# Performance work log

Hardware: AMD Instinct MI355X
Metric: run time of the kernel (lower is better)

## Reference

```python
import jax, jax.numpy as jnp
import numpy as np

EPS = 1e-09  # present in module but unused in forward math

def setup_inputs() -> dict:
    key = jax.random.key(0)
    k1, k2 = jax.random.split(key)
    n, d = 4096, 512
    outputs = jax.random.normal(k1, (n, d), dtype=jnp.float32)
    labels = jax.random.randint(k2, (n,), 0, 100, dtype=jnp.int64)
    return {"outputs": outputs, "labels": labels, "margin": 1.0}

def reference(outputs, labels, margin):
    # Pairwise squared L2 distances D[i,j] = ||x_i - x_j||^2 via expansion.
    sq = jnp.sum(outputs * outputs, axis=-1)                     # [n]
    D = sq[:, None] + sq[None, :] - 2.0 * (outputs @ outputs.T)  # [n, n]
    D = jnp.maximum(D, 0.0)
    same = (labels[:, None] == labels[None, :])                  # [n, n] bool; includes diagonal
    zn1 = jnp.sum(same)
    zn2 = same.size - zn1
    sum1 = jnp.sum(jnp.where(same, D, 0.0))
    sum2 = jnp.sum(jnp.where(same, 0.0, jnp.maximum(0.0, margin - D)))
    return 0.5 * (sum1 / zn1 + sum2 / zn2)
```

## Files before the change

kernel.cpp:

```cpp
#include <hip/hip_runtime.h>
#include <stdint.h>

#define NROWS 4096
#define DIM   512
#define BK    32
#define TILE  128
#define NBLK  32
#define NPAIR 528
#define KT    (DIM / BK)

typedef float f32x4 __attribute__((ext_vector_type(4)));
typedef short s16x8 __attribute__((ext_vector_type(8)));

#define OFF_XB   0u
#define OFF_SQ   (NROWS * DIM * 2u)
#define OFF_LAB  (OFF_SQ + NROWS * 4u)
#define OFF_ACC  (OFF_LAB + NROWS * 4u)

__device__ __forceinline__ unsigned short f2bf(float f) {
  unsigned u = __float_as_uint(f);
  return (unsigned short)((u + 0x7FFFu + ((u >> 16) & 1u)) >> 16);
}

typedef __attribute__((address_space(1))) unsigned int glb_uint;
typedef __attribute__((address_space(3))) unsigned int lds_uint;

__device__ __forceinline__ void gl2lds16(const void* g, void* l) {
  __builtin_amdgcn_global_load_lds(
      (glb_uint*)(uintptr_t)g,
      (lds_uint*)(unsigned int)(uintptr_t)l,
      16, 0, 0);
}

__global__ __launch_bounds__(256) void prep_kernel(
    const float* __restrict__ X, const long long* __restrict__ lab,
    unsigned short* __restrict__ Xb, float* __restrict__ sq,
    int* __restrict__ labi, float* __restrict__ accum)
{
  int t = threadIdx.x;
  int gid = blockIdx.x * 256 + t;
  if (gid < 4) accum[gid] = 0.0f;
  if (gid < NROWS) labi[gid] = (int)lab[gid];

  int wave = t >> 6, lane = t & 63;
  int row = blockIdx.x * 4 + wave;
  const float4* Xr = (const float4*)(X + (size_t)row * DIM);
  float4 a = Xr[lane * 2];
  float4 b = Xr[lane * 2 + 1];

  uint4 pk;
  pk.x = (unsigned)f2bf(a.x) | ((unsigned)f2bf(a.y) << 16);
  pk.y = (unsigned)f2bf(a.z) | ((unsigned)f2bf(a.w) << 16);
  pk.z = (unsigned)f2bf(b.x) | ((unsigned)f2bf(b.y) << 16);
  pk.w = (unsigned)f2bf(b.z) | ((unsigned)f2bf(b.w) << 16);
  *(uint4*)(Xb + (size_t)row * DIM + lane * 8) = pk;

  float s = a.x*a.x + a.y*a.y + a.z*a.z + a.w*a.w
          + b.x*b.x + b.y*b.y + b.z*b.z + b.w*b.w;
  #pragma unroll
  for (int off = 32; off; off >>= 1) s += __shfl_down(s, off, 64);
  if (lane == 0) sq[row] = s;
}

__global__ __launch_bounds__(256) void pair_kernel(
    const unsigned short* __restrict__ Xb, const float* __restrict__ sq,
    const int* __restrict__ labi, const float* __restrict__ marginp,
    float* __restrict__ accum, float* __restrict__ out)
{
  __shared__ unsigned short As[2][TILE * BK];
  __shared__ unsigned short Bs[2][TILE * BK];
  __shared__ float sRow[TILE], sCol[TILE];
  __shared__ int   lRow[TILE], lCol[TILE];
  __shared__ float rs1[4], rs2[4];
  __shared__ int   rc[4];

  int t = threadIdx.x;

  int rem = blockIdx.x, bi = 0;
  while (rem >= (NBLK - bi)) { rem -= (NBLK - bi); bi++; }
  int bj = bi + rem;

  if (t < TILE) {
    sRow[t] = sq[bi * TILE + t];
    lRow[t] = labi[bi * TILE + t];
  } else {
    int u = t - TILE;
    sCol[u] = sq[bj * TILE + u];
    lCol[u] = labi[bj * TILE + u];
  }

  int wave = t >> 6, lane = t & 63;
  int quad = lane >> 4, ml = lane & 15;
  int waveRow = (wave >> 1) * 64, waveCol = (wave & 1) * 64;

  f32x4 acc[4][4] = {};

  const int r0 = t >> 2;
  const int g  = (t & 3) ^ ((t >> 3) & 3);
  const size_t gA0 = (size_t)(bi * TILE +      r0) * DIM + g * 8;
  const size_t gA1 = (size_t)(bi * TILE + 64 + r0) * DIM + g * 8;
  const size_t gB0 = (size_t)(bj * TILE +      r0) * DIM + g * 8;
  const size_t gB1 = (size_t)(bj * TILE + 64 + r0) * DIM + g * 8;
  const int ldst = t * 8;

  const int slot = quad ^ ((ml >> 1) & 3);

  gl2lds16(Xb + gA0, (void*)(As[0] + ldst));
  gl2lds16(Xb + gA1, (void*)(As[0] + 2048 + ldst));
  gl2lds16(Xb + gB0, (void*)(Bs[0] + ldst));
  gl2lds16(Xb + gB1, (void*)(Bs[0] + 2048 + ldst));

  for (int kt = 0; kt < KT; ++kt) {
    int cur = kt & 1;
    __syncthreads();

    if (kt + 1 < KT) {
      size_t ko = (size_t)(kt + 1) * BK;
      gl2lds16(Xb + gA0 + ko, (void*)(As[cur ^ 1] + ldst));
      gl2lds16(Xb + gA1 + ko, (void*)(As[cur ^ 1] + 2048 + ldst));
      gl2lds16(Xb + gB0 + ko, (void*)(Bs[cur ^ 1] + ldst));
      gl2lds16(Xb + gB1 + ko, (void*)(Bs[cur ^ 1] + 2048 + ldst));
    }

    const s16x8* Ap = (const s16x8*)As[cur];
    const s16x8* Bp = (const s16x8*)Bs[cur];
    s16x8 af[4], bfr[4];
    #pragma unroll
    for (int r = 0; r < 4; ++r) {
      int row = waveRow + r * 16 + ml;
      af[r] = Ap[row * 4 + slot];
    }
    #pragma unroll
    for (int c = 0; c < 4; ++c) {
      int col = waveCol + c * 16 + ml;
      bfr[c] = Bp[col * 4 + slot];
    }

    #pragma unroll
    for (int r = 0; r < 4; ++r)
      #pragma unroll
      for (int c = 0; c < 4; ++c)
        acc[r][c] = __builtin_amdgcn_mfma_f32_16x16x32_bf16(af[r], bfr[c], acc[r][c], 0, 0, 0);
  }

  float margin = *marginp;
  float s1 = 0.f, s2 = 0.f;
  int cnt = 0;
  #pragma unroll
  for (int c = 0; c < 4; ++c) {
    int col = waveCol + c * 16 + ml;
    float sqc = sCol[col];
    int lc = lCol[col];
    #pragma unroll
    for (int r = 0; r < 4; ++r) {
      int rbase = waveRow + r * 16 + quad * 4;
      #pragma unroll
      for (int i = 0; i < 4; ++i) {
        int row = rbase + i;
        float d = sRow[row] + sqc - 2.0f * acc[r][c][i];
        d = fmaxf(d, 0.0f);
        if (lRow[row] == lc) { s1 += d; cnt++; }
        else                 { s2 += fmaxf(margin - d, 0.0f); }
      }
    }
  }

  #pragma unroll
  for (int off = 32; off; off >>= 1) {
    s1  += __shfl_down(s1, off, 64);
    s2  += __shfl_down(s2, off, 64);
    cnt += __shfl_down(cnt, off, 64);
  }
  if (lane == 0) { rs1[wave] = s1; rs2[wave] = s2; rc[wave] = cnt; }
  __syncthreads();
  if (t == 0) {
    float f = (bi == bj) ? 1.f : 2.f;
    float S1 = 0.f, S2 = 0.f;
    int C = 0;
    for (int w = 0; w < 4; ++w) { S1 += rs1[w]; S2 += rs2[w]; C += rc[w]; }
    atomicAdd(&accum[0], S1 * f);
    atomicAdd(&accum[1], S2 * f);
    atomicAdd((unsigned*)accum + 2, (unsigned)C * (unsigned)((bi == bj) ? 1 : 2));
    __threadfence();
    unsigned prev = atomicAdd((unsigned*)accum + 3, 1u);
    if (prev == NPAIR - 1) {
      float s1v = atomicAdd(&accum[0], 0.0f);
      float s2v = atomicAdd(&accum[1], 0.0f);
      unsigned c1 = atomicAdd((unsigned*)accum + 2, 0u);
      double zn1 = (double)c1;
      double zn2 = (double)NROWS * (double)NROWS - zn1;
      out[0] = (float)(0.5 * ((double)s1v / zn1 + (double)s2v / zn2));
    }
  }
}

extern "C" void kernel_launch(void* const* d_in, const int* in_sizes, int n_in,
                              void* d_out, int out_size, void* d_ws, size_t ws_size,
                              hipStream_t stream) {
  const float*     X      = (const float*)d_in[0];
  const long long* lab    = (const long long*)d_in[1];
  const float*     margin = (const float*)d_in[2];
  float*           out    = (float*)d_out;

  char* ws = (char*)d_ws;
  unsigned short* Xb   = (unsigned short*)(ws + OFF_XB);
  float*          sq   = (float*)(ws + OFF_SQ);
  int*            labi = (int*)(ws + OFF_LAB);
  float*          accum= (float*)(ws + OFF_ACC);

  prep_kernel<<<NROWS / 4, 256, 0, stream>>>(X, lab, Xb, sq, labi, accum);
  pair_kernel<<<NPAIR, 256, 0, stream>>>(Xb, sq, labi, margin, accum, out);
}
```

Baseline: 102.8 us.

## Load MFMA fragments directly from global memory and switch to fp16 inputs

```diff
diff --git a/kernel.cpp b/kernel.cpp
--- a/kernel.cpp
+++ b/kernel.cpp
@@ -1,40 +1,25 @@
 #include <hip/hip_runtime.h>
+#include <hip/hip_fp16.h>
 #include <stdint.h>
 
 #define NROWS 4096
 #define DIM   512
-#define BK    32
 #define TILE  128
 #define NBLK  32
 #define NPAIR 528
-#define KT    (DIM / BK)
+#define KSTEPS 16
 
-typedef float f32x4 __attribute__((ext_vector_type(4)));
-typedef short s16x8 __attribute__((ext_vector_type(8)));
+typedef float    f32x4 __attribute__((ext_vector_type(4)));
+typedef _Float16 f16x8 __attribute__((ext_vector_type(8)));
 
-#define OFF_XB   0u
+#define OFF_XH   0u
 #define OFF_SQ   (NROWS * DIM * 2u)
 #define OFF_LAB  (OFF_SQ + NROWS * 4u)
 #define OFF_ACC  (OFF_LAB + NROWS * 4u)
 
-__device__ __forceinline__ unsigned short f2bf(float f) {
-  unsigned u = __float_as_uint(f);
-  return (unsigned short)((u + 0x7FFFu + ((u >> 16) & 1u)) >> 16);
-}
-
-typedef __attribute__((address_space(1))) unsigned int glb_uint;
-typedef __attribute__((address_space(3))) unsigned int lds_uint;
-
-__device__ __forceinline__ void gl2lds16(const void* g, void* l) {
-  __builtin_amdgcn_global_load_lds(
-      (glb_uint*)(uintptr_t)g,
-      (lds_uint*)(unsigned int)(uintptr_t)l,
-      16, 0, 0);
-}
-
 __global__ __launch_bounds__(256) void prep_kernel(
     const float* __restrict__ X, const long long* __restrict__ lab,
-    unsigned short* __restrict__ Xb, float* __restrict__ sq,
+    unsigned short* __restrict__ Xh, float* __restrict__ sq,
     int* __restrict__ labi, float* __restrict__ accum)
 {
   int t = threadIdx.x;
@@ -49,11 +34,11 @@
   float4 b = Xr[lane * 2 + 1];
 
   uint4 pk;
-  pk.x = (unsigned)f2bf(a.x) | ((unsigned)f2bf(a.y) << 16);
-  pk.y = (unsigned)f2bf(a.z) | ((unsigned)f2bf(a.w) << 16);
-  pk.z = (unsigned)f2bf(b.x) | ((unsigned)f2bf(b.y) << 16);
-  pk.w = (unsigned)f2bf(b.z) | ((unsigned)f2bf(b.w) << 16);
-  *(uint4*)(Xb + (size_t)row * DIM + lane * 8) = pk;
+  pk.x = (unsigned)__half_as_ushort(__float2half(a.x)) | ((unsigned)__half_as_ushort(__float2half(a.y)) << 16);
+  pk.y = (unsigned)__half_as_ushort(__float2half(a.z)) | ((unsigned)__half_as_ushort(__float2half(a.w)) << 16);
+  pk.z = (unsigned)__half_as_ushort(__float2half(b.x)) | ((unsigned)__half_as_ushort(__float2half(b.y)) << 16);
+  pk.w = (unsigned)__half_as_ushort(__float2half(b.z)) | ((unsigned)__half_as_ushort(__float2half(b.w)) << 16);
+  *(uint4*)(Xh + (size_t)row * DIM + lane * 8) = pk;
 
   float s = a.x*a.x + a.y*a.y + a.z*a.z + a.w*a.w
           + b.x*b.x + b.y*b.y + b.z*b.z + b.w*b.w;
@@ -62,13 +47,11 @@
   if (lane == 0) sq[row] = s;
 }
 
-__global__ __launch_bounds__(256) void pair_kernel(
-    const unsigned short* __restrict__ Xb, const float* __restrict__ sq,
+__global__ __launch_bounds__(256, 2) void pair_kernel(
+    const unsigned short* __restrict__ Xh, const float* __restrict__ sq,
     const int* __restrict__ labi, const float* __restrict__ marginp,
     float* __restrict__ accum, float* __restrict__ out)
 {
-  __shared__ unsigned short As[2][TILE * BK];
-  __shared__ unsigned short Bs[2][TILE * BK];
   __shared__ float sRow[TILE], sCol[TILE];
   __shared__ int   lRow[TILE], lCol[TILE];
   __shared__ float rs1[4], rs2[4];
@@ -93,55 +76,33 @@
   int quad = lane >> 4, ml = lane & 15;
   int waveRow = (wave >> 1) * 64, waveCol = (wave & 1) * 64;
 
+  const f16x8* ap[4];
+  const f16x8* bp[4];
+  #pragma unroll
+  for (int r = 0; r < 4; ++r) {
+    int grow = bi * TILE + waveRow + r * 16 + ml;
+    int gcol = bj * TILE + waveCol + r * 16 + ml;
+    ap[r] = (const f16x8*)(Xh + (size_t)grow * DIM + quad * 8);
+    bp[r] = (const f16x8*)(Xh + (size_t)gcol * DIM + quad * 8);
+  }
+
   f32x4 acc[4][4] = {};
 
-  const int r0 = t >> 2;
-  const int g  = (t & 3) ^ ((t >> 3) & 3);
-  const size_t gA0 = (size_t)(bi * TILE +      r0) * DIM + g * 8;
-  const size_t gA1 = (size_t)(bi * TILE + 64 + r0) * DIM + g * 8;
-  const size_t gB0 = (size_t)(bj * TILE +      r0) * DIM + g * 8;
-  const size_t gB1 = (size_t)(bj * TILE + 64 + r0) * DIM + g * 8;
-  const int ldst = t * 8;
-
-  const int slot = quad ^ ((ml >> 1) & 3);
-
-  gl2lds16(Xb + gA0, (void*)(As[0] + ldst));
-  gl2lds16(Xb + gA1, (void*)(As[0] + 2048 + ldst));
-  gl2lds16(Xb + gB0, (void*)(Bs[0] + ldst));
-  gl2lds16(Xb + gB1, (void*)(Bs[0] + 2048 + ldst));
-
-  for (int kt = 0; kt < KT; ++kt) {
-    int cur = kt & 1;
-    __syncthreads();
-
-    if (kt + 1 < KT) {
-      size_t ko = (size_t)(kt + 1) * BK;
-      gl2lds16(Xb + gA0 + ko, (void*)(As[cur ^ 1] + ldst));
-      gl2lds16(Xb + gA1 + ko, (void*)(As[cur ^ 1] + 2048 + ldst));
-      gl2lds16(Xb + gB0 + ko, (void*)(Bs[cur ^ 1] + ldst));
-      gl2lds16(Xb + gB1 + ko, (void*)(Bs[cur ^ 1] + 2048 + ldst));
-    }
-
-    const s16x8* Ap = (const s16x8*)As[cur];
-    const s16x8* Bp = (const s16x8*)Bs[cur];
-    s16x8 af[4], bfr[4];
+  #pragma unroll
+  for (int ks = 0; ks < KSTEPS; ++ks) {
+    f16x8 af[4], bf[4];
     #pragma unroll
-    for (int r = 0; r < 4; ++r) {
-      int row = waveRow + r * 16 + ml;
-      af[r] = Ap[row * 4 + slot];
-    }
+    for (int r = 0; r < 4; ++r) af[r] = ap[r][ks * 4];
     #pragma unroll
-    for (int c = 0; c < 4; ++c) {
-      int col = waveCol + c * 16 + ml;
-      bfr[c] = Bp[col * 4 + slot];
-    }
-
+    for (int c = 0; c < 4; ++c) bf[c] = bp[c][ks * 4];
     #pragma unroll
     for (int r = 0; r < 4; ++r)
       #pragma unroll
       for (int c = 0; c < 4; ++c)
-        acc[r][c] = __builtin_amdgcn_mfma_f32_16x16x32_bf16(af[r], bfr[c], acc[r][c], 0, 0, 0);
+        acc[r][c] = __builtin_amdgcn_mfma_f32_16x16x32_f16(af[r], bf[c], acc[r][c], 0, 0, 0);
   }
+
+  __syncthreads();
 
   float margin = *marginp;
   float s1 = 0.f, s2 = 0.f;
@@ -203,11 +164,11 @@
   float*           out    = (float*)d_out;
 
   char* ws = (char*)d_ws;
-  unsigned short* Xb   = (unsigned short*)(ws + OFF_XB);
+  unsigned short* Xh   = (unsigned short*)(ws + OFF_XH);
   float*          sq   = (float*)(ws + OFF_SQ);
   int*            labi = (int*)(ws + OFF_LAB);
   float*          accum= (float*)(ws + OFF_ACC);
 
-  prep_kernel<<<NROWS / 4, 256, 0, stream>>>(X, lab, Xb, sq, labi, accum);
-  pair_kernel<<<NPAIR, 256, 0, stream>>>(Xb, sq, labi, margin, accum, out);
+  prep_kernel<<<NROWS / 4, 256, 0, stream>>>(X, lab, Xh, sq, labi, accum);
+  pair_kernel<<<NPAIR, 256, 0, stream>>>(Xh, sq, labi, margin, accum, out);
 }
```

Measured after the change: 132.4 us. 28.7% more time.
